# Kernel optimization log

Hardware: AMD Instinct MI355X
Metric: run time of the kernel (lower is better)

Reference implementation:

```python
import jax, jax.numpy as jnp
import numpy as np

N_ATOMS = 100_000  # number of center atoms
K = 16             # neighbors per atom within cutoff (uniform for static shapes)


def setup_inputs() -> dict:
    # pair_i: sorted center-atom index per neighbor pair, K neighbors per atom.
    pair_i = jnp.repeat(jnp.arange(N_ATOMS, dtype=jnp.int32), K)  # [N_ATOMS*K]
    return {"pair_i": pair_i, "n_atoms": N_ATOMS, "max_neighbors": K}


def reference(pair_i, n_atoms, max_neighbors):
    """Segmented combinations: for each atom's contiguous neighbor block,
    emit all unique (j,k) pair-index combinations, exactly matching the
    torch.combinations lexicographic order of the original Python loop.
    Assumes uniform neighbor count == max_neighbors (as built in setup)."""
    ones = jnp.ones_like(pair_i)
    counts = jax.ops.segment_sum(ones, pair_i, num_segments=n_atoms)  # [n_atoms]
    starts = jnp.cumsum(counts) - counts                              # block offsets (prefix sum)

    # within-block combination template, shared by all atoms
    pu, pv = jnp.triu_indices(max_neighbors, k=1)  # [T_per], T_per = K*(K-1)/2
    t_per = pu.shape[0]

    idx_i = jnp.repeat(jnp.arange(n_atoms, dtype=pair_i.dtype), t_per)          # [n_atoms*T_per]
    idx_j = (starts[:, None] + pu[None, :]).reshape(-1).astype(pair_i.dtype)    # [n_atoms*T_per]
    idx_k = (starts[:, None] + pv[None, :]).reshape(-1).astype(pair_i.dtype)    # [n_atoms*T_per]
    return idx_i, idx_j, idx_k
```

## Files before the change

### kernel.cpp

```cpp
#include <hip/hip_runtime.h>


constexpr int K      = 16;
constexpr int T_PER  = K * (K - 1) / 2;
constexpr int GROUPS = T_PER / 4;
constexpr int BLK    = 256;
constexpr int ITERS  = 12;
constexpr int CHUNK  = BLK * ITERS;

typedef int iv4 __attribute__((ext_vector_type(4)));

struct Tbl { unsigned u[GROUPS]; unsigned v[GROUPS]; };
constexpr Tbl make_tbl() {
    Tbl t{};
    int idx = 0;
    for (int a = 0; a < K; ++a)
        for (int b = a + 1; b < K; ++b) {
            t.u[idx / 4] |= (unsigned)a << ((idx % 4) * 8);
            t.v[idx / 4] |= (unsigned)b << ((idx % 4) * 8);
            ++idx;
        }
    return t;
}
__device__ constexpr Tbl TBL = make_tbl();

__global__ void starts_kernel(const int* __restrict__ pair_i, int* __restrict__ starts,
                              int n_atoms, int m) {
    int a = blockIdx.x * blockDim.x + threadIdx.x;
    if (a >= n_atoms) return;
    int lo = 0, hi = m;
    while (lo < hi) {
        int mid = (lo + hi) >> 1;
        if (pair_i[mid] < a) lo = mid + 1; else hi = mid;
    }
    starts[a] = lo;
}

__global__ __launch_bounds__(BLK)
void gen_split(const int* __restrict__ starts, int* __restrict__ out,
               int per_arr_groups) {
    const int s  = blockIdx.x % 3;
    const int b  = blockIdx.x / 3;
    const int g0 = b * CHUNK;
    if (g0 >= per_arr_groups) return;

    iv4* __restrict__ o = (iv4*)out + (size_t)s * per_arr_groups;
    const bool full = (g0 + CHUNK) <= per_arr_groups;

    if (s == 0) {
        if (full) {
            #pragma unroll
            for (int k = 0; k < ITERS; ++k) {
                const int g    = g0 + k * BLK + (int)threadIdx.x;
                const int atom = g / GROUPS;
                iv4 v; v[0] = atom; v[1] = atom; v[2] = atom; v[3] = atom;
                o[g] = v;
            }
        } else {
            for (int g = g0 + (int)threadIdx.x; g < per_arr_groups; g += BLK) {
                const int atom = g / GROUPS;
                iv4 v; v[0] = atom; v[1] = atom; v[2] = atom; v[3] = atom;
                o[g] = v;
            }
        }
        return;
    }

    __shared__ int      s_st[CHUNK / GROUPS + 2];
    __shared__ unsigned s_tb[GROUPS];
    const int gend = full ? (g0 + CHUNK) : per_arr_groups;
    const int a0   = g0 / GROUPS;
    const int a1   = (gend - 1) / GROUPS;
    const int na   = a1 - a0 + 1;
    if ((int)threadIdx.x < na)     s_st[threadIdx.x] = starts[a0 + (int)threadIdx.x];
    if ((int)threadIdx.x < GROUPS) s_tb[threadIdx.x] = (s == 1 ? TBL.u : TBL.v)[threadIdx.x];
    __syncthreads();

    if (full) {
        #pragma unroll
        for (int k = 0; k < ITERS; ++k) {
            const int g     = g0 + k * BLK + (int)threadIdx.x;
            const int atom  = g / GROUPS;
            const int r     = g - atom * GROUPS;
            const int start = s_st[atom - a0];
            const unsigned ub = s_tb[r];
            iv4 v;
            v[0] = start + (int)(ub & 0xff);
            v[1] = start + (int)((ub >> 8)  & 0xff);
            v[2] = start + (int)((ub >> 16) & 0xff);
            v[3] = start + (int)((ub >> 24) & 0xff);
            o[g] = v;
        }
    } else {
        for (int g = g0 + (int)threadIdx.x; g < gend; g += BLK) {
            const int atom  = g / GROUPS;
            const int r     = g - atom * GROUPS;
            const int start = s_st[atom - a0];
            const unsigned ub = s_tb[r];
            iv4 v;
            v[0] = start + (int)(ub & 0xff);
            v[1] = start + (int)((ub >> 8)  & 0xff);
            v[2] = start + (int)((ub >> 16) & 0xff);
            v[3] = start + (int)((ub >> 24) & 0xff);
            o[g] = v;
        }
    }
}

extern "C" void kernel_launch(void* const* d_in, const int* in_sizes, int n_in,
                              void* d_out, int out_size, void* d_ws, size_t ws_size,
                              hipStream_t stream) {
    const int* pair_i  = (const int*)d_in[0];
    const int  m       = in_sizes[0];
    const int  n_atoms = m / K;

    int* out = (int*)d_out;
    const int per_arr_groups = n_atoms * GROUPS;

    int* starts = (int*)d_ws;
    {
        const int b1 = 256;
        starts_kernel<<<(n_atoms + b1 - 1) / b1, b1, 0, stream>>>(pair_i, starts, n_atoms, m);
    }

    const int nbs  = (per_arr_groups + CHUNK - 1) / CHUNK;
    gen_split<<<3 * nbs, BLK, 0, stream>>>(starts, out, per_arr_groups);
}
```

Measured before the change: 158.9 us.

## Fuse starts binary search into generator kernel and use nontemporal stores

Removes the separate starts kernel and computes each block's atom start offsets inline by binary search over pair_i, eliminating one launch and the workspace round-trip. It also switches the output writes to nontemporal stores so the large streaming output bypasses cache retention, and halves ITERS to launch more, smaller blocks. In exchange, starts are recomputed redundantly by both the u and v block families, and the serial binary search now sits ahead of the stores in each block.

```diff
diff --git a/kernel.cpp b/kernel.cpp
--- a/kernel.cpp
+++ b/kernel.cpp
@@ -5,7 +5,7 @@
 constexpr int T_PER  = K * (K - 1) / 2;
 constexpr int GROUPS = T_PER / 4;
 constexpr int BLK    = 256;
-constexpr int ITERS  = 12;
+constexpr int ITERS  = 6;
 constexpr int CHUNK  = BLK * ITERS;
 
 typedef int iv4 __attribute__((ext_vector_type(4)));
@@ -24,21 +24,9 @@
 }
 __device__ constexpr Tbl TBL = make_tbl();
 
-__global__ void starts_kernel(const int* __restrict__ pair_i, int* __restrict__ starts,
-                              int n_atoms, int m) {
-    int a = blockIdx.x * blockDim.x + threadIdx.x;
-    if (a >= n_atoms) return;
-    int lo = 0, hi = m;
-    while (lo < hi) {
-        int mid = (lo + hi) >> 1;
-        if (pair_i[mid] < a) lo = mid + 1; else hi = mid;
-    }
-    starts[a] = lo;
-}
-
 __global__ __launch_bounds__(BLK)
-void gen_split(const int* __restrict__ starts, int* __restrict__ out,
-               int per_arr_groups) {
+void gen_fused(const int* __restrict__ pair_i, int* __restrict__ out,
+               int m, int per_arr_groups) {
     const int s  = blockIdx.x % 3;
     const int b  = blockIdx.x / 3;
     const int g0 = b * CHUNK;
@@ -46,40 +34,49 @@
 
     iv4* __restrict__ o = (iv4*)out + (size_t)s * per_arr_groups;
     const bool full = (g0 + CHUNK) <= per_arr_groups;
+    const int  gend = full ? (g0 + CHUNK) : per_arr_groups;
 
     if (s == 0) {
         if (full) {
             #pragma unroll
-            for (int k = 0; k < ITERS; ++k) {
-                const int g    = g0 + k * BLK + (int)threadIdx.x;
+            for (int k2 = 0; k2 < ITERS; ++k2) {
+                const int g    = g0 + k2 * BLK + (int)threadIdx.x;
                 const int atom = g / GROUPS;
                 iv4 v; v[0] = atom; v[1] = atom; v[2] = atom; v[3] = atom;
-                o[g] = v;
+                __builtin_nontemporal_store(v, &o[g]);
             }
         } else {
-            for (int g = g0 + (int)threadIdx.x; g < per_arr_groups; g += BLK) {
+            for (int g = g0 + (int)threadIdx.x; g < gend; g += BLK) {
                 const int atom = g / GROUPS;
                 iv4 v; v[0] = atom; v[1] = atom; v[2] = atom; v[3] = atom;
-                o[g] = v;
+                __builtin_nontemporal_store(v, &o[g]);
             }
         }
         return;
     }
 
-    __shared__ int      s_st[CHUNK / GROUPS + 2];
+    __shared__ int      s_st[CHUNK / GROUPS + 3];
     __shared__ unsigned s_tb[GROUPS];
-    const int gend = full ? (g0 + CHUNK) : per_arr_groups;
-    const int a0   = g0 / GROUPS;
-    const int a1   = (gend - 1) / GROUPS;
-    const int na   = a1 - a0 + 1;
-    if ((int)threadIdx.x < na)     s_st[threadIdx.x] = starts[a0 + (int)threadIdx.x];
-    if ((int)threadIdx.x < GROUPS) s_tb[threadIdx.x] = (s == 1 ? TBL.u : TBL.v)[threadIdx.x];
+    const int a0 = g0 / GROUPS;
+    const int a1 = (gend - 1) / GROUPS;
+    const int na = a1 - a0 + 1;
+    if ((int)threadIdx.x < na) {
+        const int a = a0 + (int)threadIdx.x;
+        int lo = 0, hi = m;
+        while (lo < hi) {
+            const int mid = (lo + hi) >> 1;
+            if (pair_i[mid] < a) lo = mid + 1; else hi = mid;
+        }
+        s_st[threadIdx.x] = lo;
+    }
+    if ((int)threadIdx.x < GROUPS)
+        s_tb[threadIdx.x] = (s == 1 ? TBL.u : TBL.v)[threadIdx.x];
     __syncthreads();
 
     if (full) {
         #pragma unroll
-        for (int k = 0; k < ITERS; ++k) {
-            const int g     = g0 + k * BLK + (int)threadIdx.x;
+        for (int k2 = 0; k2 < ITERS; ++k2) {
+            const int g     = g0 + k2 * BLK + (int)threadIdx.x;
             const int atom  = g / GROUPS;
             const int r     = g - atom * GROUPS;
             const int start = s_st[atom - a0];
@@ -89,7 +86,7 @@
             v[1] = start + (int)((ub >> 8)  & 0xff);
             v[2] = start + (int)((ub >> 16) & 0xff);
             v[3] = start + (int)((ub >> 24) & 0xff);
-            o[g] = v;
+            __builtin_nontemporal_store(v, &o[g]);
         }
     } else {
         for (int g = g0 + (int)threadIdx.x; g < gend; g += BLK) {
@@ -102,7 +99,7 @@
             v[1] = start + (int)((ub >> 8)  & 0xff);
             v[2] = start + (int)((ub >> 16) & 0xff);
             v[3] = start + (int)((ub >> 24) & 0xff);
-            o[g] = v;
+            __builtin_nontemporal_store(v, &o[g]);
         }
     }
 }
@@ -117,12 +114,6 @@
     int* out = (int*)d_out;
     const int per_arr_groups = n_atoms * GROUPS;
 
-    int* starts = (int*)d_ws;
-    {
-        const int b1 = 256;
-        starts_kernel<<<(n_atoms + b1 - 1) / b1, b1, 0, stream>>>(pair_i, starts, n_atoms, m);
-    }
-
-    const int nbs  = (per_arr_groups + CHUNK - 1) / CHUNK;
-    gen_split<<<3 * nbs, BLK, 0, stream>>>(starts, out, per_arr_groups);
+    const int nbs = (per_arr_groups + CHUNK - 1) / CHUNK;
+    gen_fused<<<3 * nbs, BLK, 0, stream>>>(pair_i, out, m, per_arr_groups);
 }
```

Result: slower. 167.3 us (+5.3%).
